# Optimization experiments

Measured on AMD Instinct MI355X. Metric: run time of the kernel, lower is better.

The kernel has to match this reference:

```python
import jax, jax.numpy as jnp
import numpy as np

B, Q, H, W, C = 2, 8192, 64, 64, 64
C9 = C * 9
EPS = 1e-6


def _mlp(x, params):
    # gelu MLP, no activation on last layer (matches repo mlp)
    for Wm, b in params[:-1]:
        x = jax.nn.gelu(x @ Wm + b)
    Wl, bl = params[-1]
    return x @ Wl + bl


def _make_coord(h, w):
    # pixel-center coords in (-1,1); channel 0 = row dim, channel 1 = col dim
    hs = -1.0 + (2.0 * jnp.arange(h, dtype=jnp.float32) + 1.0) / h
    ws = -1.0 + (2.0 * jnp.arange(w, dtype=jnp.float32) + 1.0) / w
    return jnp.stack(jnp.meshgrid(hs, ws, indexing='ij'), axis=0)  # (2,h,w)


def _nearest_gather(feat, coord):
    # F.grid_sample(mode='nearest', align_corners=False) on a (B,1,q,2) grid.
    # feat (B,C,H,W); coord (B,q,2) with [...,0] indexing H, [...,1] indexing W
    h, w = feat.shape[-2], feat.shape[-1]
    ih = jnp.clip(jnp.round((coord[..., 0] + 1.0) * h / 2.0 - 0.5), 0, h - 1).astype(jnp.int32)
    iw = jnp.clip(jnp.round((coord[..., 1] + 1.0) * w / 2.0 - 0.5), 0, w - 1).astype(jnp.int32)
    return jax.vmap(lambda f, a, b: f[:, a, b].T)(feat, ih, iw)  # (B,q,C)


def _unfold3(feat):
    # F.unfold(feat, 3, padding=1).view(B, C*9, H, W): channel-major, kernel row-major
    b, c, h, w = feat.shape
    p = jnp.pad(feat, ((0, 0), (0, 0), (1, 1), (1, 1)))
    patches = jnp.stack([p[:, :, i:i + h, j:j + w] for i in range(3) for j in range(3)], axis=2)
    return patches.reshape(b, c * 9, h, w)


def _forward(inp, coord, scale, enc_w, enc_b, iw0, ib0, iw1, ib1, iw2, ib2,
             sw0, sb0, sw1, sb1, ww0, wb0, ww1, wb1):
    # encoder (stand-in conv3x3, 3 -> C feature channels)
    feat = jax.lax.conv_general_dilated(inp, enc_w, (1, 1), 'SAME',
                                        dimension_numbers=('NCHW', 'OIHW', 'NCHW'))
    feat = feat + enc_b[None, :, None, None]
    feat = _unfold3(feat)  # (B, C*9, H, W)
    bsz, cf, h, w = feat.shape
    fcoord = jnp.broadcast_to(_make_coord(h, w)[None], (bsz, 2, h, w))
    dims = jnp.array([h, w], dtype=feat.dtype)

    tx = (h - 1) / (1.0 - scale[:, 0, 0])  # (B,)
    ty = (w - 1) / (1.0 - scale[:, 0, 1])
    rx, ry = 1.0 / tx, 1.0 / ty
    scale_tok = scale * dims  # (B,q,2)

    imnet_p = [(iw0, ib0), (iw1, ib1), (iw2, ib2)]
    score_p = [(sw0, sb0), (sw1, sb1)]
    weight_p = [(ww0, wb0), (ww1, wb1)]

    preds = []
    for vx in (-1, 1):
        for vy in (-1, 1):
            shift = jnp.stack([vx * rx + EPS, vy * ry + EPS], axis=-1)[:, None, :]  # (B,1,2)
            c = jnp.clip(coord + shift, -1.0 + 1e-6, 1.0 - 1e-6)
            value = _nearest_gather(feat, c)      # (B,q,C*9)
            coord_k = _nearest_gather(fcoord, c)  # (B,q,2)
            rel = (coord - coord_k) * dims        # (B,q,2)
            score = _mlp(rel, score_p)            # (B,q,1) -> broadcast over 3
            mlp_in = jnp.concatenate([rel, scale_tok], axis=-1)  # (B,q,4)
            wmat = _mlp(mlp_in, imnet_p).reshape(bsz, -1, cf, 3)  # (B,q,C*9,3)
            preds.append(jnp.einsum('bqc,bqck->bqk', value, wmat) + score)
    stacked = jnp.stack(preds, axis=-1)  # (B,q,3,4)
    return _mlp(stacked, weight_p)[..., 0]  # (B,q,3)


def setup_inputs() -> dict:
    key = jax.random.key(0)
    ks = jax.random.split(key, 16)
    f32 = jnp.float32

    def wi(k, shape, fan_in):
        return jax.random.normal(k, shape, f32) / np.float32(np.sqrt(fan_in))

    return {
        'inp': jax.random.normal(ks[0], (B, 3, H, W), f32),
        'coord': jax.random.uniform(ks[1], (B, Q, 2), f32, -1.0 + 1e-4, 1.0 - 1e-4),
        'scale': jax.random.uniform(ks[2], (B, Q, 2), f32, 0.01, 0.05),
        'enc_w': wi(ks[3], (C, 3, 3, 3), 27),
        'enc_b': jnp.zeros((C,), f32),
        'iw0': wi(ks[4], (4, 256), 4), 'ib0': jnp.zeros((256,), f32),
        'iw1': wi(ks[5], (256, 256), 256), 'ib1': jnp.zeros((256,), f32),
        'iw2': wi(ks[6], (256, C9 * 3), 256), 'ib2': jnp.zeros((C9 * 3,), f32),
        'sw0': wi(ks[7], (2, 256), 2), 'sb0': jnp.zeros((256,), f32),
        'sw1': wi(ks[8], (256, 1), 256), 'sb1': jnp.zeros((1,), f32),
        'ww0': wi(ks[9], (4, 256), 4), 'wb0': jnp.zeros((256,), f32),
        'ww1': wi(ks[10], (256, 1), 256), 'wb1': jnp.zeros((1,), f32),
    }


def reference(inp, coord, scale, enc_w, enc_b, iw0, ib0, iw1, ib1, iw2, ib2,
              sw0, sb0, sw1, sb1, ww0, wb0, ww1, wb1):
    return _forward(inp, coord, scale, enc_w, enc_b, iw0, ib0, iw1, ib1, iw2, ib2,
                    sw0, sb0, sw1, sb1, ww0, wb0, ww1, wb1)
```

## Files before the change

kernel.cpp:

```cpp
#include <hip/hip_runtime.h>

#define QN 8192
#define CCH 64
#define NROW 65536
#define MR 64
#define NBLK (NROW / MR)
#define H0S 264

typedef _Float16 f16x8 __attribute__((ext_vector_type(8)));
typedef _Float16 f16x4 __attribute__((ext_vector_type(4)));
typedef float f32x4 __attribute__((ext_vector_type(4)));

__device__ __forceinline__ float gelu_f(float x) {
    float x2 = x * x;
    float tt = fmaf(0.044715f, x2, 1.0f);
    float e = __expf(1.5957691216f * x * tt);
    float r = __builtin_amdgcn_rcpf(1.0f + e);
    return x - x * r;
}

__global__ __launch_bounds__(256) void k_pre(const float* __restrict__ inp,
                                             const float* __restrict__ ew,
                                             const float* __restrict__ eb,
                                             const float* __restrict__ coord,
                                             const float* __restrict__ scale,
                                             const float* __restrict__ sw0,
                                             const float* __restrict__ sb0,
                                             const float* __restrict__ sw1,
                                             const float* __restrict__ sb1,
                                             const float* __restrict__ iw1,
                                             const float* __restrict__ iw2,
                                             const float* __restrict__ ib2,
                                             float* __restrict__ featpad,
                                             float4* __restrict__ mlp_in,
                                             int2* __restrict__ ihiw,
                                             float* __restrict__ scoreg,
                                             _Float16* __restrict__ w1tp,
                                             _Float16* __restrict__ w2tp,
                                             float* __restrict__ b2p) {
    const int bb = blockIdx.x;
    const int tt0 = threadIdx.x;
    if (bb < 2178) {
        __shared__ float s_ew[1728];
        for (int i = tt0; i < 1728; i += 256) s_ew[i] = ew[i];
        __syncthreads();
        int idx = bb * 256 + tt0;
        const int total = 2 * 66 * 66 * CCH;
        if (idx >= total) return;
        int o = idx & 63; int pix = idx >> 6;
        int xx = pix % 66; int t2 = pix / 66;
        int yy = t2 % 66;  int b = t2 / 66;
        int y = yy - 1, x = xx - 1;
        float acc = 0.0f;
        if (y >= 0 && y < 64 && x >= 0 && x < 64) {
            acc = eb[o];
            for (int i = 0; i < 3; ++i) {
                const float* ip = inp + ((b * 3 + i) * 64) * 64;
                const float* wp = s_ew + (o * 3 + i) * 9;
                #pragma unroll
                for (int ky = 0; ky < 3; ++ky) {
                    int sy = y + ky - 1;
                    if (sy < 0 || sy > 63) continue;
                    #pragma unroll
                    for (int kx = 0; kx < 3; ++kx) {
                        int sx = x + kx - 1;
                        if (sx < 0 || sx > 63) continue;
                        acc += ip[sy * 64 + sx] * wp[ky * 3 + kx];
                    }
                }
            }
        }
        featpad[idx] = acc;
    } else if (bb < 2434) {
        int row = (bb - 2178) * 256 + tt0;
        int v = row & 3;
        int bq = row >> 2;
        int b = bq >> 13;
        float c0 = coord[bq * 2 + 0], c1 = coord[bq * 2 + 1];
        float s0 = scale[bq * 2 + 0], s1 = scale[bq * 2 + 1];
        float s00 = scale[(b * QN) * 2 + 0];
        float s01 = scale[(b * QN) * 2 + 1];
        float rx = (1.0f - s00) / 63.0f;
        float ry = (1.0f - s01) / 63.0f;
        float vx = (v & 2) ? 1.0f : -1.0f;
        float vy = (v & 1) ? 1.0f : -1.0f;
        float cc0 = c0 + vx * rx + 1e-6f;
        float cc1 = c1 + vy * ry + 1e-6f;
        cc0 = fminf(fmaxf(cc0, -1.0f + 1e-6f), 1.0f - 1e-6f);
        cc1 = fminf(fmaxf(cc1, -1.0f + 1e-6f), 1.0f - 1e-6f);
        int ih = (int)rintf((cc0 + 1.0f) * 32.0f - 0.5f);
        int iw = (int)rintf((cc1 + 1.0f) * 32.0f - 0.5f);
        ih = min(max(ih, 0), 63);
        iw = min(max(iw, 0), 63);
        float ck0 = (2.0f * (float)ih + 1.0f) / 64.0f - 1.0f;
        float ck1 = (2.0f * (float)iw + 1.0f) / 64.0f - 1.0f;
        float rel0 = (c0 - ck0) * 64.0f;
        float rel1 = (c1 - ck1) * 64.0f;
        mlp_in[row] = make_float4(rel0, rel1, s0 * 64.0f, s1 * 64.0f);
        ihiw[row] = make_int2(ih, iw);
        float sc = sb1[0];
        #pragma unroll 4
        for (int t2 = 0; t2 < 256; ++t2) {
            float h = gelu_f(fmaf(rel0, sw0[t2], fmaf(rel1, sw0[256 + t2], sb0[t2])));
            sc = fmaf(h, sw1[t2], sc);
        }
        scoreg[row] = sc;
    } else {
        int idx = (bb - 2434) * 256 + tt0;
        if (idx < 442368) {
            int j = idx & 7, ln = (idx >> 3) & 63, kf = (idx >> 9) & 7, tl = idx >> 12;
            int np = tl * 16 + (ln & 15);
            int kk = kf * 32 + (ln >> 4) * 8 + j;
            int k_out = np / 576;
            int rem = np - 576 * k_out;
            int tap = rem >> 6, cch = rem & 63;
            int n = (cch * 9 + tap) * 3 + k_out;
            w2tp[idx] = (_Float16)iw2[kk * 1728 + n];
            if (kf == 0 && j == 0 && (ln >> 4) == 0) b2p[np] = ib2[n];
        } else {
            int i2 = idx - 442368;
            int j = i2 & 7, ln = (i2 >> 3) & 63, kf = (i2 >> 9) & 7, ct = i2 >> 12;
            int col = ct * 16 + (ln & 15);
            int kk = kf * 32 + (ln >> 4) * 8 + j;
            w1tp[i2] = (_Float16)iw1[kk * 256 + col];
        }
    }
}

__global__ __launch_bounds__(256, 2) void k_fused(const float* __restrict__ featpad,
                                                  const float4* __restrict__ mlp_in,
                                                  const int2* __restrict__ ihiw,
                                                  const float* __restrict__ iw0,
                                                  const float* __restrict__ ib0,
                                                  const _Float16* __restrict__ w1tp,
                                                  const float* __restrict__ ib1,
                                                  const _Float16* __restrict__ w2tp,
                                                  const float* __restrict__ b2p,
                                                  const float* __restrict__ scoreg,
                                                  const float* __restrict__ ww0,
                                                  const float* __restrict__ wb0,
                                                  const float* __restrict__ ww1,
                                                  const float* __restrict__ wb1,
                                                  float* __restrict__ out) {
    __shared__ __align__(16) char pool[576 * 64 * 2];
    _Float16* s_h0   = (_Float16*)pool;
    _Float16* s_valT = (_Float16*)pool;
    __shared__ float4 s_min[MR];
    __shared__ int    s_base[MR];
    __shared__ int    s_dtab[9];
    __shared__ float  s_pred[MR][3];
    __shared__ float  s_score[MR];
    __shared__ float  s_wred[48][4];

    const int t = threadIdx.x;
    const int wave = t >> 6, lane = t & 63, quad = lane >> 4, l15 = lane & 15;
    const int rowbase = blockIdx.x * MR;

    if (t < MR) {
        int row = rowbase + t;
        s_min[t] = mlp_in[row];
        s_score[t] = scoreg[row];
        int b = row >> 15;
        int2 p = ihiw[row];
        s_base[t] = ((b * 66 + p.x) * 66 + p.y) * 64;
    }
    if (t < 9) { int di = t / 3; s_dtab[t] = (di * 66 + (t - 3 * di)) * 64; }
    if (t < MR * 3) s_pred[t / 3][t % 3] = 0.0f;
    __syncthreads();

    {
        float w0 = iw0[t], w1 = iw0[256 + t], w2 = iw0[512 + t], w3 = iw0[768 + t];
        float bb = ib0[t];
        #pragma unroll 4
        for (int r = 0; r < MR; ++r) {
            float4 m = s_min[r];
            s_h0[r * H0S + t] =
                (_Float16)gelu_f(fmaf(m.x, w0, fmaf(m.y, w1, fmaf(m.z, w2, fmaf(m.w, w3, bb)))));
        }
    }
    __syncthreads();

    f16x8 hX[4], hY[4];
    {
        const _Float16* wp = w1tp + (size_t)((wave * 4) * 8) * 512 + lane * 8;
        #pragma unroll
        for (int kf = 0; kf < 4; ++kf) hX[kf] = *(const f16x8*)(wp + kf * 512);
    }

    f16x8 a[4][8];
    #pragma unroll
    for (int rt = 0; rt < 4; ++rt)
        #pragma unroll
        for (int kf = 0; kf < 8; ++kf)
            a[rt][kf] = *(const f16x8*)(s_h0 + (rt * 16 + l15) * H0S + kf * 32 + quad * 8);
    __syncthreads();

    #pragma unroll 1
    for (int c = 0; c < 4; ++c) {
        int ct = wave * 4 + c;
        {
            const _Float16* wp = w1tp + (size_t)(ct * 8 + 4) * 512 + lane * 8;
            #pragma unroll
            for (int kf = 0; kf < 4; ++kf) hY[kf] = *(const f16x8*)(wp + kf * 512);
        }
        f32x4 acc[4] = {{0.f,0.f,0.f,0.f},{0.f,0.f,0.f,0.f},{0.f,0.f,0.f,0.f},{0.f,0.f,0.f,0.f}};
        #pragma unroll
        for (int kf = 0; kf < 4; ++kf)
            #pragma unroll
            for (int rt = 0; rt < 4; ++rt)
                acc[rt] = __builtin_amdgcn_mfma_f32_16x16x32_f16(a[rt][kf], hX[kf], acc[rt], 0, 0, 0);
        if (c < 3) {
            const _Float16* wp = w1tp + (size_t)((ct + 1) * 8) * 512 + lane * 8;
            #pragma unroll
            for (int kf = 0; kf < 4; ++kf) hX[kf] = *(const f16x8*)(wp + kf * 512);
        }
        #pragma unroll
        for (int kf = 0; kf < 4; ++kf)
            #pragma unroll
            for (int rt = 0; rt < 4; ++rt)
                acc[rt] = __builtin_amdgcn_mfma_f32_16x16x32_f16(a[rt][kf + 4], hY[kf], acc[rt], 0, 0, 0);
        int col = ct * 16 + l15;
        float bias = ib1[col];
        #pragma unroll
        for (int rt = 0; rt < 4; ++rt)
            #pragma unroll
            for (int reg = 0; reg < 4; ++reg)
                s_h0[(rt * 16 + quad * 4 + reg) * H0S + col] = (_Float16)gelu_f(acc[rt][reg] + bias);
    }
    __syncthreads();

    #pragma unroll
    for (int rt = 0; rt < 4; ++rt)
        #pragma unroll
        for (int kf = 0; kf < 8; ++kf)
            a[rt][kf] = *(const f16x8*)(s_h0 + (rt * 16 + l15) * H0S + kf * 32 + quad * 8);
    __syncthreads();

    const int tbase = wave * 27;
    f16x8 bfX[4], bfY[4];
    {
        const _Float16* wp = w2tp + (size_t)(tbase * 8) * 512 + lane * 8;
        #pragma unroll
        for (int kf = 0; kf < 4; ++kf) bfX[kf] = *(const f16x8*)(wp + kf * 512);
    }

    #pragma unroll 1
    for (int g4 = 0; g4 < 9; ++g4) {
        float4 v[4];
        #pragma unroll
        for (int u = 0; u < 4; ++u) {
            int c4 = wave + (g4 * 4 + u) * 4;
            int tap = c4 >> 4;
            int cch0 = (c4 & 15) << 2;
            v[u] = *(const float4*)(featpad + s_base[lane] + s_dtab[tap] + cch0);
        }
        #pragma unroll
        for (int u = 0; u < 4; ++u) {
            int c4 = wave + (g4 * 4 + u) * 4;
            int cfp = c4 << 2;
            s_valT[(cfp + 0) * 64 + (lane ^ (((cfp + 0) & 7) << 3))] = (_Float16)v[u].x;
            s_valT[(cfp + 1) * 64 + (lane ^ (((cfp + 1) & 7) << 3))] = (_Float16)v[u].y;
            s_valT[(cfp + 2) * 64 + (lane ^ (((cfp + 2) & 7) << 3))] = (_Float16)v[u].z;
            s_valT[(cfp + 3) * 64 + (lane ^ (((cfp + 3) & 7) << 3))] = (_Float16)v[u].w;
        }
    }
    __syncthreads();

    const int kt0 = tbase / 36;
    int bsplit = (kt0 + 1) * 36 - tbase; if (bsplit > 27) bsplit = 27;
    const int ktB = (tbase + 26) / 36;
    const int swz = (l15 & 7) << 3;

    float pA[4][4];
    #pragma unroll
    for (int rt = 0; rt < 4; ++rt)
        #pragma unroll
        for (int rg = 0; rg < 4; ++rg) pA[rt][rg] = 0.f;

    float bv;
    #pragma unroll 1
    for (int i = 0; i < 27; ++i) {
        int ti = tbase + i;
        {
            const _Float16* wp = w2tp + (size_t)(ti * 8 + 4) * 512 + lane * 8;
            #pragma unroll
            for (int kf = 0; kf < 4; ++kf) bfY[kf] = *(const f16x8*)(wp + kf * 512);
            bv = b2p[ti * 16 + l15];
        }
        f32x4 acc[4] = {{0.f,0.f,0.f,0.f},{0.f,0.f,0.f,0.f},{0.f,0.f,0.f,0.f},{0.f,0.f,0.f,0.f}};
        #pragma unroll
        for (int kf = 0; kf < 4; ++kf)
            #pragma unroll
            for (int rt = 0; rt < 4; ++rt)
                acc[rt] = __builtin_amdgcn_mfma_f32_16x16x32_f16(a[rt][kf], bfX[kf], acc[rt], 0, 0, 0);
        if (i < 26) {
            const _Float16* wp = w2tp + (size_t)((ti + 1) * 8) * 512 + lane * 8;
            #pragma unroll
            for (int kf = 0; kf < 4; ++kf) bfX[kf] = *(const f16x8*)(wp + kf * 512);
        }
        #pragma unroll
        for (int kf = 0; kf < 4; ++kf)
            #pragma unroll
            for (int rt = 0; rt < 4; ++rt)
                acc[rt] = __builtin_amdgcn_mfma_f32_16x16x32_f16(a[rt][kf + 4], bfY[kf], acc[rt], 0, 0, 0);
        int cf36 = ti - (ti / 36) * 36;
        int cfp = cf36 * 16 + l15;
        const _Float16* vbase = s_valT + cfp * 64;
        #pragma unroll
        for (int rt = 0; rt < 4; ++rt) {
            f16x4 vv = *(const f16x4*)(vbase + ((rt * 16 + quad * 4) ^ swz));
            #pragma unroll
            for (int rg = 0; rg < 4; ++rg) {
                float s = acc[rt][rg] + bv;
                pA[rt][rg] = fmaf(s, (float)vv[rg], pA[rt][rg]);
            }
        }
        if (i == bsplit - 1) {
            #pragma unroll
            for (int rt = 0; rt < 4; ++rt)
                #pragma unroll
                for (int rg = 0; rg < 4; ++rg) {
                    float x = pA[rt][rg];
                    #pragma unroll
                    for (int m = 1; m < 16; m <<= 1) x += __shfl_xor(x, m, 64);
                    if (l15 == 0) atomicAdd(&s_pred[rt * 16 + quad * 4 + rg][kt0], x);
                    pA[rt][rg] = 0.f;
                }
        }
    }
    #pragma unroll
    for (int rt = 0; rt < 4; ++rt)
        #pragma unroll
        for (int rg = 0; rg < 4; ++rg) {
            float x = pA[rt][rg];
            #pragma unroll
            for (int m = 1; m < 16; m <<= 1) x += __shfl_xor(x, m, 64);
            if (l15 == 0) atomicAdd(&s_pred[rt * 16 + quad * 4 + rg][ktB], x);
        }
    __syncthreads();

    if (t < 192) {
        int o = t >> 2, sub = t & 3;
        int bql = o / 3, k = o - 3 * bql;
        float x0 = s_pred[bql * 4 + 0][k] + s_score[bql * 4 + 0];
        float x1 = s_pred[bql * 4 + 1][k] + s_score[bql * 4 + 1];
        float x2 = s_pred[bql * 4 + 2][k] + s_score[bql * 4 + 2];
        float x3 = s_pred[bql * 4 + 3][k] + s_score[bql * 4 + 3];
        float acc = 0.0f;
        int j0 = sub * 64;
        #pragma unroll 4
        for (int j = j0; j < j0 + 64; ++j) {
            float h = gelu_f(fmaf(x0, ww0[j], fmaf(x1, ww0[256 + j],
                          fmaf(x2, ww0[512 + j], fmaf(x3, ww0[768 + j], wb0[j])))));
            acc = fmaf(h, ww1[j], acc);
        }
        s_wred[o][sub] = acc;
    }
    __syncthreads();
    if (t < 48) {
        int bql = t / 3, k = t - 3 * bql;
        float r2 = s_wred[t][0] + s_wred[t][1] + s_wred[t][2] + s_wred[t][3] + wb1[0];
        out[(blockIdx.x * 16 + bql) * 3 + k] = r2;
    }
}

extern "C" void kernel_launch(void* const* d_in, const int* in_sizes, int n_in,
                              void* d_out, int out_size, void* d_ws, size_t ws_size,
                              hipStream_t stream) {
    const float* inp   = (const float*)d_in[0];
    const float* coord = (const float*)d_in[1];
    const float* scale = (const float*)d_in[2];
    const float* ew    = (const float*)d_in[3];
    const float* eb    = (const float*)d_in[4];
    const float* iw0   = (const float*)d_in[5];
    const float* ib0   = (const float*)d_in[6];
    const float* iw1   = (const float*)d_in[7];
    const float* ib1   = (const float*)d_in[8];
    const float* iw2   = (const float*)d_in[9];
    const float* ib2   = (const float*)d_in[10];
    const float* sw0   = (const float*)d_in[11];
    const float* sb0   = (const float*)d_in[12];
    const float* sw1   = (const float*)d_in[13];
    const float* sb1   = (const float*)d_in[14];
    const float* ww0   = (const float*)d_in[15];
    const float* wb0   = (const float*)d_in[16];
    const float* ww1   = (const float*)d_in[17];
    const float* wb1   = (const float*)d_in[18];
    float* out = (float*)d_out;

    char* ws = (char*)d_ws;
    float*     featpad = (float*)(ws + 0);
    float4*    mlp_in  = (float4*)(ws + 2230272);
    int2*      ihiw    = (int2*)(ws + 3278848);
    float*     scoreg  = (float*)(ws + 3803136);
    _Float16*  w1tp    = (_Float16*)(ws + 4065280);
    _Float16*  w2tp    = (_Float16*)(ws + 4196352);
    float*     b2p     = (float*)(ws + 5081088);

    k_pre<<<dim3(4418), dim3(256), 0, stream>>>(inp, ew, eb, coord, scale,
                                                sw0, sb0, sw1, sb1, iw1, iw2, ib2,
                                                featpad, mlp_in, ihiw, scoreg,
                                                w1tp, w2tp, b2p);
    k_fused<<<dim3(NBLK), dim3(256), 0, stream>>>(featpad, mlp_in, ihiw,
                                                  iw0, ib0, w1tp, ib1, w2tp, b2p,
                                                  scoreg, ww0, wb0, ww1, wb1, out);
}
```

Baseline: 240.4 us.

## Double-buffer weight fragments and prefetch layer-2 weights across the MLP layers

Replaces the single-buffered hX/hY and bfX/bfY weight fragments with two register buffer sets. Global loads for the next tile are issued a full tile ahead of the MFMAs that consume them. The layer-1 loop is fully unrolled, and its tail prefetches the first layer-2 weight tiles and bias so those loads overlap the layer-1 epilogue and the value-gather phase. The layer-2 loop is unrolled by two with a peeled final tile. This adds register pressure under launch_bounds(256,2), which risks spills or lower occupancy.

New measurement: 231.9 us. 1.04x faster.

```diff
diff --git a/kernel.cpp b/kernel.cpp
--- a/kernel.cpp
+++ b/kernel.cpp
@@ -127,6 +127,37 @@
     }
 }
 
+#define LDX1(B, CT) do { const _Float16* wp_ = w1tp + (size_t)((CT) * 8) * 512 + lane * 8;        \
+    _Pragma("unroll") for (int kf_ = 0; kf_ < 4; ++kf_) B[kf_] = *(const f16x8*)(wp_ + kf_ * 512); } while (0)
+#define LDY1(B, CT) do { const _Float16* wp_ = w1tp + (size_t)((CT) * 8 + 4) * 512 + lane * 8;    \
+    _Pragma("unroll") for (int kf_ = 0; kf_ < 4; ++kf_) B[kf_] = *(const f16x8*)(wp_ + kf_ * 512); } while (0)
+#define LDX2(B, TI) do { const _Float16* wp_ = w2tp + (size_t)((TI) * 8) * 512 + lane * 8;        \
+    _Pragma("unroll") for (int kf_ = 0; kf_ < 4; ++kf_) B[kf_] = *(const f16x8*)(wp_ + kf_ * 512); } while (0)
+#define LDY2(B, BV, TI) do { const _Float16* wp_ = w2tp + (size_t)((TI) * 8 + 4) * 512 + lane * 8;\
+    _Pragma("unroll") for (int kf_ = 0; kf_ < 4; ++kf_) B[kf_] = *(const f16x8*)(wp_ + kf_ * 512);\
+    BV = b2p[(TI) * 16 + l15]; } while (0)
+#define ZACC() do { _Pragma("unroll") for (int rt_ = 0; rt_ < 4; ++rt_)                           \
+    acc[rt_] = (f32x4){0.f, 0.f, 0.f, 0.f}; } while (0)
+#define MFMAH(B, OFS) do { _Pragma("unroll") for (int kf_ = 0; kf_ < 4; ++kf_)                    \
+    { _Pragma("unroll") for (int rt_ = 0; rt_ < 4; ++rt_)                                         \
+      acc[rt_] = __builtin_amdgcn_mfma_f32_16x16x32_f16(a[rt_][kf_ + (OFS)], B[kf_], acc[rt_], 0, 0, 0); } } while (0)
+#define H1EPI(CT) do { int col_ = (CT) * 16 + l15; float bias_ = ib1[col_];                       \
+    _Pragma("unroll") for (int rt_ = 0; rt_ < 4; ++rt_)                                           \
+      { _Pragma("unroll") for (int rg_ = 0; rg_ < 4; ++rg_)                                       \
+        s_h0[(rt_ * 16 + quad * 4 + rg_) * H0S + col_] = (_Float16)gelu_f(acc[rt_][rg_] + bias_); } } while (0)
+#define EPI3(TI, BV) do { int cf36_ = (TI) - ((TI) / 36) * 36;                                    \
+    const _Float16* vb_ = s_valT + (cf36_ * 16 + l15) * 64;                                       \
+    _Pragma("unroll") for (int rt_ = 0; rt_ < 4; ++rt_) {                                         \
+      f16x4 vv_ = *(const f16x4*)(vb_ + ((rt_ * 16 + quad * 4) ^ swz));                           \
+      _Pragma("unroll") for (int rg_ = 0; rg_ < 4; ++rg_)                                         \
+        pA[rt_][rg_] = fmaf(acc[rt_][rg_] + (BV), (float)vv_[rg_], pA[rt_][rg_]); } } while (0)
+#define FLUSH(KT) do { _Pragma("unroll") for (int rt_ = 0; rt_ < 4; ++rt_)                        \
+    { _Pragma("unroll") for (int rg_ = 0; rg_ < 4; ++rg_) {                                       \
+        float x_ = pA[rt_][rg_];                                                                  \
+        _Pragma("unroll") for (int m_ = 1; m_ < 16; m_ <<= 1) x_ += __shfl_xor(x_, m_, 64);       \
+        if (l15 == 0) atomicAdd(&s_pred[rt_ * 16 + quad * 4 + rg_][KT], x_);                      \
+        pA[rt_][rg_] = 0.f; } } } while (0)
+
 __global__ __launch_bounds__(256, 2) void k_fused(const float* __restrict__ featpad,
                                                   const float4* __restrict__ mlp_in,
                                                   const int2* __restrict__ ihiw,
@@ -180,12 +211,15 @@
     }
     __syncthreads();
 
-    f16x8 hX[4], hY[4];
-    {
-        const _Float16* wp = w1tp + (size_t)((wave * 4) * 8) * 512 + lane * 8;
-        #pragma unroll
-        for (int kf = 0; kf < 4; ++kf) hX[kf] = *(const f16x8*)(wp + kf * 512);
-    }
+    f16x8 bX0[4], bX1[4], bY0[4], bY1[4];
+    float bv0, bv1;
+    f32x4 acc[4];
+    const int w4 = wave * 4;
+    const int tbase = wave * 27;
+
+    LDX1(bX0, w4);
+    LDY1(bY0, w4);
+    LDX1(bX1, w4 + 1);
 
     f16x8 a[4][8];
     #pragma unroll
@@ -195,38 +229,26 @@
             a[rt][kf] = *(const f16x8*)(s_h0 + (rt * 16 + l15) * H0S + kf * 32 + quad * 8);
     __syncthreads();
 
-    #pragma unroll 1
-    for (int c = 0; c < 4; ++c) {
-        int ct = wave * 4 + c;
-        {
-            const _Float16* wp = w1tp + (size_t)(ct * 8 + 4) * 512 + lane * 8;
-            #pragma unroll
-            for (int kf = 0; kf < 4; ++kf) hY[kf] = *(const f16x8*)(wp + kf * 512);
-        }
-        f32x4 acc[4] = {{0.f,0.f,0.f,0.f},{0.f,0.f,0.f,0.f},{0.f,0.f,0.f,0.f},{0.f,0.f,0.f,0.f}};
-        #pragma unroll
-        for (int kf = 0; kf < 4; ++kf)
-            #pragma unroll
-            for (int rt = 0; rt < 4; ++rt)
-                acc[rt] = __builtin_amdgcn_mfma_f32_16x16x32_f16(a[rt][kf], hX[kf], acc[rt], 0, 0, 0);
-        if (c < 3) {
-            const _Float16* wp = w1tp + (size_t)((ct + 1) * 8) * 512 + lane * 8;
-            #pragma unroll
-            for (int kf = 0; kf < 4; ++kf) hX[kf] = *(const f16x8*)(wp + kf * 512);
-        }
-        #pragma unroll
-        for (int kf = 0; kf < 4; ++kf)
-            #pragma unroll
-            for (int rt = 0; rt < 4; ++rt)
-                acc[rt] = __builtin_amdgcn_mfma_f32_16x16x32_f16(a[rt][kf + 4], hY[kf], acc[rt], 0, 0, 0);
-        int col = ct * 16 + l15;
-        float bias = ib1[col];
-        #pragma unroll
-        for (int rt = 0; rt < 4; ++rt)
-            #pragma unroll
-            for (int reg = 0; reg < 4; ++reg)
-                s_h0[(rt * 16 + quad * 4 + reg) * H0S + col] = (_Float16)gelu_f(acc[rt][reg] + bias);
-    }
+    LDY1(bY1, w4 + 1);
+    ZACC(); MFMAH(bX0, 0);
+    LDX1(bX0, w4 + 2);
+    MFMAH(bY0, 4);
+    H1EPI(w4);
+    LDY1(bY0, w4 + 2);
+    ZACC(); MFMAH(bX1, 0);
+    LDX1(bX1, w4 + 3);
+    MFMAH(bY1, 4);
+    H1EPI(w4 + 1);
+    LDY1(bY1, w4 + 3);
+    ZACC(); MFMAH(bX0, 0);
+    LDX2(bX0, tbase);
+    MFMAH(bY0, 4);
+    H1EPI(w4 + 2);
+    LDY2(bY0, bv0, tbase);
+    ZACC(); MFMAH(bX1, 0);
+    LDX2(bX1, tbase + 1);
+    MFMAH(bY1, 4);
+    H1EPI(w4 + 3);
     __syncthreads();
 
     #pragma unroll
@@ -235,14 +257,6 @@
         for (int kf = 0; kf < 8; ++kf)
             a[rt][kf] = *(const f16x8*)(s_h0 + (rt * 16 + l15) * H0S + kf * 32 + quad * 8);
     __syncthreads();
-
-    const int tbase = wave * 27;
-    f16x8 bfX[4], bfY[4];
-    {
-        const _Float16* wp = w2tp + (size_t)(tbase * 8) * 512 + lane * 8;
-        #pragma unroll
-        for (int kf = 0; kf < 4; ++kf) bfX[kf] = *(const f16x8*)(wp + kf * 512);
-    }
 
     #pragma unroll 1
     for (int g4 = 0; g4 < 9; ++g4) {
@@ -277,66 +291,29 @@
         #pragma unroll
         for (int rg = 0; rg < 4; ++rg) pA[rt][rg] = 0.f;
 
-    float bv;
     #pragma unroll 1
-    for (int i = 0; i < 27; ++i) {
+    for (int p = 0; p < 13; ++p) {
+        int i = 2 * p;
         int ti = tbase + i;
-        {
-            const _Float16* wp = w2tp + (size_t)(ti * 8 + 4) * 512 + lane * 8;
-            #pragma unroll
-            for (int kf = 0; kf < 4; ++kf) bfY[kf] = *(const f16x8*)(wp + kf * 512);
-            bv = b2p[ti * 16 + l15];
-        }
-        f32x4 acc[4] = {{0.f,0.f,0.f,0.f},{0.f,0.f,0.f,0.f},{0.f,0.f,0.f,0.f},{0.f,0.f,0.f,0.f}};
-        #pragma unroll
-        for (int kf = 0; kf < 4; ++kf)
-            #pragma unroll
-            for (int rt = 0; rt < 4; ++rt)
-                acc[rt] = __builtin_amdgcn_mfma_f32_16x16x32_f16(a[rt][kf], bfX[kf], acc[rt], 0, 0, 0);
-        if (i < 26) {
-            const _Float16* wp = w2tp + (size_t)((ti + 1) * 8) * 512 + lane * 8;
-            #pragma unroll
-            for (int kf = 0; kf < 4; ++kf) bfX[kf] = *(const f16x8*)(wp + kf * 512);
-        }
-        #pragma unroll
-        for (int kf = 0; kf < 4; ++kf)
-            #pragma unroll
-            for (int rt = 0; rt < 4; ++rt)
-                acc[rt] = __builtin_amdgcn_mfma_f32_16x16x32_f16(a[rt][kf + 4], bfY[kf], acc[rt], 0, 0, 0);
-        int cf36 = ti - (ti / 36) * 36;
-        int cfp = cf36 * 16 + l15;
-        const _Float16* vbase = s_valT + cfp * 64;
-        #pragma unroll
-        for (int rt = 0; rt < 4; ++rt) {
-            f16x4 vv = *(const f16x4*)(vbase + ((rt * 16 + quad * 4) ^ swz));
-            #pragma unroll
-            for (int rg = 0; rg < 4; ++rg) {
-                float s = acc[rt][rg] + bv;
-                pA[rt][rg] = fmaf(s, (float)vv[rg], pA[rt][rg]);
-            }
-        }
-        if (i == bsplit - 1) {
-            #pragma unroll
-            for (int rt = 0; rt < 4; ++rt)
-                #pragma unroll
-                for (int rg = 0; rg < 4; ++rg) {
-                    float x = pA[rt][rg];
-                    #pragma unroll
-                    for (int m = 1; m < 16; m <<= 1) x += __shfl_xor(x, m, 64);
-                    if (l15 == 0) atomicAdd(&s_pred[rt * 16 + quad * 4 + rg][kt0], x);
-                    pA[rt][rg] = 0.f;
-                }
-        }
-    }
-    #pragma unroll
-    for (int rt = 0; rt < 4; ++rt)
-        #pragma unroll
-        for (int rg = 0; rg < 4; ++rg) {
-            float x = pA[rt][rg];
-            #pragma unroll
-            for (int m = 1; m < 16; m <<= 1) x += __shfl_xor(x, m, 64);
-            if (l15 == 0) atomicAdd(&s_pred[rt * 16 + quad * 4 + rg][ktB], x);
-        }
+        LDY2(bY1, bv1, ti + 1);
+        ZACC(); MFMAH(bX0, 0);
+        LDX2(bX0, ti + 2);
+        MFMAH(bY0, 4);
+        EPI3(ti, bv0);
+        if (i == bsplit - 1) FLUSH(kt0);
+        LDY2(bY0, bv0, ti + 2);
+        ZACC(); MFMAH(bX1, 0);
+        if (p < 12) LDX2(bX1, ti + 3);
+        MFMAH(bY1, 4);
+        EPI3(ti + 1, bv1);
+        if (i + 1 == bsplit - 1) FLUSH(kt0);
+    }
+    {
+        ZACC(); MFMAH(bX0, 0); MFMAH(bY0, 4);
+        EPI3(tbase + 26, bv0);
+        if (26 == bsplit - 1) FLUSH(kt0);
+    }
+    FLUSH(ktB);
     __syncthreads();
 
     if (t < 192) {
@@ -346,15 +323,15 @@
         float x1 = s_pred[bql * 4 + 1][k] + s_score[bql * 4 + 1];
         float x2 = s_pred[bql * 4 + 2][k] + s_score[bql * 4 + 2];
         float x3 = s_pred[bql * 4 + 3][k] + s_score[bql * 4 + 3];
-        float acc = 0.0f;
+        float acc2 = 0.0f;
         int j0 = sub * 64;
         #pragma unroll 4
         for (int j = j0; j < j0 + 64; ++j) {
             float h = gelu_f(fmaf(x0, ww0[j], fmaf(x1, ww0[256 + j],
                           fmaf(x2, ww0[512 + j], fmaf(x3, ww0[768 + j], wb0[j])))));
-            acc = fmaf(h, ww1[j], acc);
-        }
-        s_wred[o][sub] = acc;
+            acc2 = fmaf(h, ww1[j], acc2);
+        }
+        s_wred[o][sub] = acc2;
     }
     __syncthreads();
     if (t < 48) {
```
